# Performance work log

Measured on AMD Instinct MI355X. Metric: run time of the kernel, lower is better.

## Reference

```python
import jax, jax.numpy as jnp
import numpy as np

SAMPLE_NUM = 1024   # number of FPS centroids
RADIUS = 0.2        # ball-query radius
NEIGHBOR_NUM = 64   # max neighbors per ball


def setup_inputs() -> dict:
    key = jax.random.key(0)
    k1, k2 = jax.random.split(key)
    B, N, C = 4, 8192, 256
    xyz = jax.random.uniform(k1, (B, N, 3), dtype=jnp.float32)   # points in unit cube
    feat = jax.random.normal(k2, (B, N, C), dtype=jnp.float32)
    return {"xyz": xyz, "feat": feat}


def farthest_point_sample(xyz, K):
    """Iterative FPS. xyz: (B,N,3) -> indices (B,K). Deterministic start at index 0
    (stands in for pytorch3d's random_start_point for reproducibility)."""
    B, N, _ = xyz.shape
    start = jnp.zeros((B,), dtype=jnp.int32)
    min_d = jnp.full((B, N), jnp.inf, dtype=xyz.dtype)

    def step(carry, _):
        min_d, cur = carry
        sel = jnp.take_along_axis(xyz, cur[:, None, None], axis=1)      # (B,1,3)
        d = jnp.sum((xyz - sel) ** 2, axis=-1)                          # (B,N)
        min_d = jnp.minimum(min_d, d)
        nxt = jnp.argmax(min_d, axis=-1).astype(jnp.int32)
        return (min_d, nxt), cur

    (_, _), idxs = jax.lax.scan(step, (min_d, start), None, length=K)
    return jnp.transpose(idxs)                                          # (B,K)


def ball_query_idx(sample_xyz, xyz, radius, K):
    """For each centroid, first-K (by point index) points within radius; -1 padding.
    Matches pytorch3d ball_query index semantics."""
    B, S, _ = sample_xyz.shape
    N = xyz.shape[1]
    # squared distances via |a|^2 + |b|^2 - 2ab to avoid a (B,S,N,3) temp
    d2 = (jnp.sum(sample_xyz ** 2, -1)[:, :, None]
          + jnp.sum(xyz ** 2, -1)[:, None, :]
          - 2.0 * jnp.einsum('bsd,bnd->bsn', sample_xyz, xyz))          # (B,S,N)
    within = d2 < radius * radius
    cand = jnp.where(within, jnp.arange(N, dtype=jnp.int32), N)         # invalid -> N
    neg_topk, _ = jax.lax.top_k(-cand, K)                               # K smallest indices
    idx = -neg_topk                                                     # (B,S,K)
    return jnp.where(idx == N, -1, idx)


def reference(xyz, feat):
    B, N, C = feat.shape
    S, K = SAMPLE_NUM, NEIGHBOR_NUM
    samp_idx = farthest_point_sample(xyz, S)                            # (B,S)
    sample_xyz = jnp.take_along_axis(xyz, samp_idx[..., None], axis=1)  # (B,S,3)
    nbr_idx = ball_query_idx(sample_xyz, xyz, RADIUS, K)                # (B,S,K)
    # faithful to original gather(): -1 is replaced by idx.shape[1] == S
    idx2 = jnp.where(nbr_idx == -1, S, nbr_idx)
    neighbor_feat = jnp.take_along_axis(
        feat, idx2.reshape(B, S * K)[..., None], axis=1
    ).reshape(B, S, K, C)                                               # (B,S,K,C)
    return (sample_xyz, neighbor_feat)
```

## Files before the change

kernel.cpp:

```cpp
#include <hip/hip_runtime.h>
#include <cstdint>

#define NB   4
#define NPT  8192
#define NC   256
#define NS   1024
#define NK   64
#define FPT  32

typedef float v2f __attribute__((ext_vector_type(2)));

template <int CTRL, int RMASK>
__device__ __forceinline__ float dpp_max_step(float x) {
    const int t = __builtin_amdgcn_update_dpp(
        0, __float_as_int(x), CTRL, RMASK, 0xf, false);
    return fmaxf(x, __int_as_float(t));
}
__device__ __forceinline__ float wave_max_f32(float x) {
    x = dpp_max_step<0x111, 0xf>(x);
    x = dpp_max_step<0x112, 0xf>(x);
    x = dpp_max_step<0x114, 0xf>(x);
    x = dpp_max_step<0x118, 0xf>(x);
    x = dpp_max_step<0x142, 0xa>(x);
    x = dpp_max_step<0x143, 0xc>(x);
    return x;
}

__global__ __launch_bounds__(256, 1) void fps_kernel(
    const float* __restrict__ xyz, float* __restrict__ sample_xyz)
{
    const int b   = blockIdx.x;
    const int tid = threadIdx.x;

    __shared__ float Xs[NPT], Ys[NPT], Zs[NPT];
    __shared__ float Samp[NS * 3];
    __shared__ unsigned long long slots[3];

    const float* base = xyz + (size_t)b * NPT * 3;

    v2f px[16], py[16], pz[16], md[16];
#pragma unroll
    for (int j = 0; j < 16; ++j) {
        const int pa = tid * FPT + j;
        const int pb = tid * FPT + 16 + j;
        const float ax = base[pa * 3 + 0], ay = base[pa * 3 + 1], az = base[pa * 3 + 2];
        const float bx = base[pb * 3 + 0], by = base[pb * 3 + 1], bz = base[pb * 3 + 2];
        px[j] = (v2f){ax, bx};
        py[j] = (v2f){ay, by};
        pz[j] = (v2f){az, bz};
        md[j] = (v2f){__builtin_inff(), __builtin_inff()};
        Xs[pa] = ax; Ys[pa] = ay; Zs[pa] = az;
        Xs[pb] = bx; Ys[pb] = by; Zs[pb] = bz;
    }
    if (tid < 3) slots[tid] = 0ull;
    __syncthreads();

    int widx = 0;
    int cur = 0, nxt = 1;
    for (int s = 0; s < NS; ++s) {
        const float sx = Xs[widx];
        const float sy = Ys[widx];
        const float sz = Zs[widx];
        if (tid == 0) {
            Samp[s * 3 + 0] = sx; Samp[s * 3 + 1] = sy; Samp[s * 3 + 2] = sz;
            slots[nxt] = 0ull;
        }

        const v2f sxv = (v2f){sx, sx};
        const v2f syv = (v2f){sy, sy};
        const v2f szv = (v2f){sz, sz};

        v2f best2 = (v2f){-1.0f, -1.0f};
        int jx = 0, jy = 0;
        {
#pragma clang fp contract(off)
#pragma unroll
            for (int j = 0; j < 16; ++j) {
                const v2f dx = px[j] - sxv;
                const v2f dy = py[j] - syv;
                const v2f dz = pz[j] - szv;
                const v2f d  = (dx * dx + dy * dy) + dz * dz;
                const v2f m  = __builtin_elementwise_min(md[j], d);
                md[j] = m;
                if (m.x > best2.x) jx = j;
                if (m.y > best2.y) jy = j;
                best2 = __builtin_elementwise_max(best2, m);
            }
        }
        float    bestval;
        unsigned bestidx;
        if (best2.y > best2.x) { bestval = best2.y; bestidx = (unsigned)(tid * FPT + 16 + jy); }
        else                   { bestval = best2.x; bestidx = (unsigned)(tid * FPT + jx); }

        const float wmax = wave_max_f32(bestval);
        const float smax = __int_as_float(
            __builtin_amdgcn_readlane(__float_as_int(wmax), 63));
        const unsigned long long msk = __ballot(bestval == smax);
        const int wl = __ffsll((long long)msk) - 1;
        const unsigned widx_w =
            (unsigned)__builtin_amdgcn_readlane((int)bestidx, wl);
        if ((tid & 63) == 0) {
            const unsigned long long key =
                ((unsigned long long)__float_as_uint(smax) << 32)
                | (unsigned long long)(0xFFFFFFFFu - widx_w);
            atomicMax(&slots[cur], key);
        }
        __syncthreads();

        const unsigned long long best = slots[cur];
        widx = (int)(0xFFFFFFFFu - (unsigned)(best & 0xFFFFFFFFull));
        cur = nxt;
        nxt = (nxt == 2) ? 0 : nxt + 1;
    }

    float* o = sample_xyz + (size_t)b * NS * 3;
    for (int i = tid; i < NS * 3; i += 256) o[i] = Samp[i];
}

__global__ __launch_bounds__(256) void bq_gather_kernel(
    const float* __restrict__ xyz, const float* __restrict__ feat,
    const float* __restrict__ sample_xyz, float* __restrict__ out_feat)
{
    const int s   = blockIdx.x;
    const int b   = blockIdx.y;
    const int tid = threadIdx.x;

    __shared__ int   list[NK];
    __shared__ int   wavecnt[4];
    __shared__ float cen[3];

    if (tid < 3) cen[tid] = sample_xyz[((size_t)b * NS + s) * 3 + tid];
    __syncthreads();
    const float sx = cen[0], sy = cen[1], sz = cen[2];
    const float na = __fadd_rn(
        __fadd_rn(__fmul_rn(sx, sx), __fmul_rn(sy, sy)), __fmul_rn(sz, sz));
    const float* bxyz = xyz + (size_t)b * NPT * 3;

    int len = 0;
    for (int c0 = 0; c0 < NPT; c0 += 256) {
        const int idx = c0 + tid;
        const float x = bxyz[idx * 3 + 0];
        const float y = bxyz[idx * 3 + 1];
        const float z = bxyz[idx * 3 + 2];
        const float nb = __fadd_rn(
            __fadd_rn(__fmul_rn(x, x), __fmul_rn(y, y)), __fmul_rn(z, z));
        const float dt = __fmaf_rn(sz, z, __fmaf_rn(sy, y, __fmul_rn(sx, x)));
        const float d2 = __fsub_rn(__fadd_rn(na, nb), __fmul_rn(2.0f, dt));
        const bool within = d2 < 0.04f;

        const unsigned long long m = __ballot(within);
        const int wvq  = tid >> 6;
        const int lane = tid & 63;
        if (lane == 0) wavecnt[wvq] = __popcll(m);
        __syncthreads();
        const int w0 = wavecnt[0], w1 = wavecnt[1], w2 = wavecnt[2], w3 = wavecnt[3];
        int off = len;
        if (wvq > 0) off += w0;
        if (wvq > 1) off += w1;
        if (wvq > 2) off += w2;
        const int pre = __popcll(m & ((1ull << lane) - 1ull));
        const int pos = off + pre;
        if (within && pos < NK) list[pos] = idx;
        len += w0 + w1 + w2 + w3;
        __syncthreads();
        if (len >= NK) break;
    }
    const int llen = len < NK ? len : NK;

    const int lane = tid & 63;
    const int sub  = tid >> 6;
    const float4* fbase = (const float4*)(feat + (size_t)b * NPT * NC);
    float4* obase = (float4*)(out_feat + (((size_t)b * NS + s) * (size_t)NK) * NC);
#pragma unroll
    for (int p = 0; p < NK / 4; ++p) {
        const int k   = p * 4 + sub;
        const int row = (k < llen) ? list[k] : NS;
        const float4 v = fbase[(size_t)row * (NC / 4) + lane];
        obase[(size_t)k * (NC / 4) + lane] = v;
    }
}

extern "C" void kernel_launch(void* const* d_in, const int* in_sizes, int n_in,
                              void* d_out, int out_size, void* d_ws, size_t ws_size,
                              hipStream_t stream) {
    const float* xyz  = (const float*)d_in[0];
    const float* feat = (const float*)d_in[1];
    float* out        = (float*)d_out;
    float* sample_xyz = out;
    float* out_feat   = out + (size_t)NB * NS * 3;

    fps_kernel<<<dim3(NB), dim3(256), 0, stream>>>(xyz, sample_xyz);
    bq_gather_kernel<<<dim3(NS, NB), dim3(256), 0, stream>>>(
        xyz, feat, sample_xyz, out_feat);
}
```

Baseline: 876.6 us.

## Replace FPS per-iteration barrier and atomicMax with tagged per-wave slots and spin-wait

Measured after the change: 1.060 ms. 1.21x slower.

```diff
diff --git a/kernel.cpp b/kernel.cpp
--- a/kernel.cpp
+++ b/kernel.cpp
@@ -29,12 +29,14 @@
 __global__ __launch_bounds__(256, 1) void fps_kernel(
     const float* __restrict__ xyz, float* __restrict__ sample_xyz)
 {
-    const int b   = blockIdx.x;
-    const int tid = threadIdx.x;
+    const int b    = blockIdx.x;
+    const int tid  = threadIdx.x;
+    const int lane = tid & 63;
+    const int wv   = tid >> 6;
 
     __shared__ float Xs[NPT], Ys[NPT], Zs[NPT];
     __shared__ float Samp[NS * 3];
-    __shared__ unsigned long long slots[3];
+    __shared__ unsigned long long slots[2][4];
 
     const float* base = xyz + (size_t)b * NPT * 3;
 
@@ -52,18 +54,36 @@
         Xs[pa] = ax; Ys[pa] = ay; Zs[pa] = az;
         Xs[pb] = bx; Ys[pb] = by; Zs[pb] = bz;
     }
-    if (tid < 3) slots[tid] = 0ull;
+    if (tid == 0) {
+        slots[0][0] = ((unsigned long long)0x7F800000u << 32) | 0x00FFFFFFull;
+    }
+    if (tid < 3) slots[0][tid + 1] = 0ull;
     __syncthreads();
 
-    int widx = 0;
-    int cur = 0, nxt = 1;
     for (int s = 0; s < NS; ++s) {
+        const int par = s & 1;
+        const unsigned tag = (unsigned)s & 0xFFu;
+
+        const volatile unsigned long long* sp = slots[par];
+        unsigned long long k0, k1, k2, k3;
+        for (;;) {
+            k0 = sp[0]; k1 = sp[1]; k2 = sp[2]; k3 = sp[3];
+            const unsigned m = (((unsigned)k0 >> 24) ^ tag)
+                             | (((unsigned)k1 >> 24) ^ tag)
+                             | (((unsigned)k2 >> 24) ^ tag)
+                             | (((unsigned)k3 >> 24) ^ tag);
+            if (m == 0) break;
+        }
+        const unsigned long long kA = k0 > k1 ? k0 : k1;
+        const unsigned long long kB = k2 > k3 ? k2 : k3;
+        const unsigned long long kw = kA > kB ? kA : kB;
+        const int widx = (int)(0x00FFFFFFu - ((unsigned)kw & 0x00FFFFFFu));
+
         const float sx = Xs[widx];
         const float sy = Ys[widx];
         const float sz = Zs[widx];
         if (tid == 0) {
             Samp[s * 3 + 0] = sx; Samp[s * 3 + 1] = sy; Samp[s * 3 + 2] = sz;
-            slots[nxt] = 0ull;
         }
 
         const v2f sxv = (v2f){sx, sx};
@@ -99,20 +119,17 @@
         const int wl = __ffsll((long long)msk) - 1;
         const unsigned widx_w =
             (unsigned)__builtin_amdgcn_readlane((int)bestidx, wl);
-        if ((tid & 63) == 0) {
-            const unsigned long long key =
+
+        if (lane == 0) {
+            const unsigned ntag = (unsigned)(s + 1) & 0xFFu;
+            *(volatile unsigned long long*)&slots[par ^ 1][wv] =
                 ((unsigned long long)__float_as_uint(smax) << 32)
-                | (unsigned long long)(0xFFFFFFFFu - widx_w);
-            atomicMax(&slots[cur], key);
-        }
-        __syncthreads();
-
-        const unsigned long long best = slots[cur];
-        widx = (int)(0xFFFFFFFFu - (unsigned)(best & 0xFFFFFFFFull));
-        cur = nxt;
-        nxt = (nxt == 2) ? 0 : nxt + 1;
-    }
-
+                | ((unsigned long long)ntag << 24)
+                | (unsigned long long)(0x00FFFFFFu - widx_w);
+        }
+    }
+
+    __syncthreads();
     float* o = sample_xyz + (size_t)b * NS * 3;
     for (int i = tid; i < NS * 3; i += 256) o[i] = Samp[i];
 }
```
